# Optimization experiments

Measured on AMD Instinct MI355X. Metric: run time of the kernel, lower is better.

The kernel has to match this reference:

```python
import jax, jax.numpy as jnp
import numpy as np


def setup_inputs() -> dict:
    key = jax.random.key(0)
    ks = jax.random.split(key, 8)
    B, T, C = 4, 1024, 1024
    s = 1.0 / np.sqrt(C)
    return {
        "q": jax.random.normal(ks[0], (B, T, C), jnp.float32),
        "k": jax.random.normal(ks[1], (B, T, C), jnp.float32),
        "v": jax.random.normal(ks[2], (B, T, C), jnp.float32),
        "Wq": jax.random.normal(ks[3], (C, C), jnp.float32) * s,
        "Wk": jax.random.normal(ks[4], (C, C), jnp.float32) * s,
        "Wv": jax.random.normal(ks[5], (C, C), jnp.float32) * s,
        "Wp": jax.random.normal(ks[6], (C, C), jnp.float32) * s,
        "bp": jnp.zeros((C,), jnp.float32),
        "n_head": 16,
        "kernel_size": 16,
    }


def reference(q, k, v, Wq, Wk, Wv, Wp, bp, n_head, kernel_size):
    B, T, C = q.shape
    H = n_head
    D = C // H

    def split_heads(x, W):
        # nn.Linear applies x @ W.T
        return (x @ W.T).reshape(B, T, H, D).transpose(0, 2, 1, 3)  # (B,H,T,D)

    qp = split_heads(q, Wq)
    kp = split_heads(k, Wk)
    vp = split_heads(v, Wv)

    # Faithful to the torch double loop: wei[b,h,i,j] = sum over feature dims
    # d in [max(0, j-ks), min(T, j+ks)) (clipped to [0,D)) of qp[b,h,i,d]*kp[b,h,i,d] / sqrt(D).
    # Both windows index sequence position i; the window slides over the head_dim axis.
    p = qp * kp / jnp.sqrt(jnp.asarray(D, qp.dtype))          # (B,H,T,D)
    cs = jnp.cumsum(p, axis=-1)
    cs = jnp.concatenate([jnp.zeros(cs.shape[:-1] + (1,), cs.dtype), cs], axis=-1)  # (B,H,T,D+1)
    j = jnp.arange(T)
    start = jnp.clip(j - kernel_size, 0, D)                   # (T,)
    end = jnp.clip(jnp.minimum(j + kernel_size, T), 0, D)     # (T,)
    wei = cs[..., end] - cs[..., start]                       # (B,H,T,T): windowed partial dot of row i

    attn = jax.nn.softmax(wei, axis=-1)
    out = jnp.einsum("bhts,bhsd->bhtd", attn, vp)             # (B,H,T,D)
    out = out.transpose(0, 2, 1, 3).reshape(B, T, C)
    out = out @ Wp.T + bp
    # dropout is identity in eval mode
    return out
```

## Files before the change

kernel.cpp:

```cpp
#include <hip/hip_runtime.h>
#include <hip/hip_bf16.h>
#include <stdint.h>


typedef __bf16 bf16x8 __attribute__((ext_vector_type(8)));
typedef float f32x4 __attribute__((ext_vector_type(4)));

#define AS1(p) ((__attribute__((address_space(1))) void*)(p))
#define AS3(p) ((__attribute__((address_space(3))) void*)(p))

__global__ __launch_bounds__(256) void cvt_kernel(
    const float* __restrict__ q, const float* __restrict__ k,
    const float* __restrict__ v, const float* __restrict__ Wq,
    const float* __restrict__ Wk, const float* __restrict__ Wv,
    const float* __restrict__ Wp,
    ushort4* __restrict__ qkv_bf, ushort4* __restrict__ w_bf)
{
  int idx = blockIdx.x * 256 + threadIdx.x;
  const float* src; ushort4* dst; int i;
  if (idx < 3145728) {
    int which = idx >> 20; i = idx & 1048575;
    src = which == 0 ? q : which == 1 ? k : v;
    dst = qkv_bf + (size_t)which * 1048576 + i;
  } else {
    int w = idx - 3145728; int which = w >> 18; i = w & 262143;
    src = which == 0 ? Wq : which == 1 ? Wk : which == 2 ? Wv : Wp;
    dst = w_bf + w;
  }
  float4 val = ((const float4*)src)[i];
  union { ushort4 u; __hip_bfloat16 h[4]; } c;
  c.h[0] = __float2bfloat16(val.x); c.h[1] = __float2bfloat16(val.y);
  c.h[2] = __float2bfloat16(val.z); c.h[3] = __float2bfloat16(val.w);
  dst[0] = c.u;
}

template <typename OutT>
__device__ __forceinline__ void gemm_tile128(
    const __hip_bfloat16* __restrict__ A, const __hip_bfloat16* __restrict__ Bw,
    OutT* __restrict__ C, const float* __restrict__ bias)
{
  const int N = 1024, K = 1024;
  __shared__ __align__(16) __hip_bfloat16 As[2][128 * 32];
  __shared__ __align__(16) __hip_bfloat16 Bs[2][128 * 32];
  const int t = threadIdx.x;
  const int wv = t >> 6, lane = t & 63;
  const int wRow = (wv >> 1) * 64, wCol = (wv & 1) * 64;
  const int mrow = lane & 15, kq = lane >> 4;

  f32x4 acc[4][4] = {};

  for (int k0 = 0; k0 < K; k0 += 64) {
    __syncthreads();
#pragma unroll
    for (int half = 0; half < 2; ++half)
#pragma unroll
      for (int tI = 0; tI < 2; ++tI) {
        int chunk = wv * 2 + tI;
        int byteOff = chunk * 1024 + lane * 16;
        int row = byteOff >> 6;
        int colEl = (byteOff & 63) >> 1;
        const __hip_bfloat16* ga = A + (size_t)row * K + k0 + half * 32 + colEl;
        __builtin_amdgcn_global_load_lds(AS1((void*)ga), AS3(&As[half][chunk * 512]), 16, 0, 0);
        const __hip_bfloat16* gb = Bw + (size_t)row * K + k0 + half * 32 + colEl;
        __builtin_amdgcn_global_load_lds(AS1((void*)gb), AS3(&Bs[half][chunk * 512]), 16, 0, 0);
      }
    __syncthreads();

#pragma unroll
    for (int half = 0; half < 2; ++half) {
      bf16x8 af[4], bf[4];
#pragma unroll
      for (int mi = 0; mi < 4; ++mi)
        af[mi] = *(const bf16x8*)&As[half][(wRow + mi * 16 + mrow) * 32 + kq * 8];
#pragma unroll
      for (int ni = 0; ni < 4; ++ni)
        bf[ni] = *(const bf16x8*)&Bs[half][(wCol + ni * 16 + mrow) * 32 + kq * 8];
#pragma unroll
      for (int mi = 0; mi < 4; ++mi)
#pragma unroll
        for (int ni = 0; ni < 4; ++ni)
          acc[mi][ni] = __builtin_amdgcn_mfma_f32_16x16x32_bf16(af[mi], bf[ni], acc[mi][ni], 0, 0, 0);
    }
  }

#pragma unroll
  for (int mi = 0; mi < 4; ++mi)
#pragma unroll
    for (int ni = 0; ni < 4; ++ni)
#pragma unroll
      for (int r = 0; r < 4; ++r) {
        int row = wRow + mi * 16 + kq * 4 + r;
        int col = wCol + ni * 16 + mrow;
        float val = acc[mi][ni][r];
        if (bias) val += bias[col];
        if constexpr (__is_same(OutT, __hip_bfloat16))
          C[(size_t)row * N + col] = __float2bfloat16(val);
        else
          C[(size_t)row * N + col] = val;
      }
}

__global__ __launch_bounds__(256) void qkv_gemm_kernel(
    const __hip_bfloat16* __restrict__ QKVbf, const __hip_bfloat16* __restrict__ Wbf,
    __hip_bfloat16* __restrict__ QKVp)
{
  int l = blockIdx.x;
  int n = l / 96, mm = l % 96, z = mm >> 5, m = mm & 31;
  gemm_tile128<__hip_bfloat16>(
      QKVbf + (size_t)z * 4194304 + (size_t)m * 131072,
      Wbf + (size_t)z * 1048576 + (size_t)n * 131072,
      QKVp + (size_t)z * 4194304 + (size_t)m * 131072 + n * 128, nullptr);
}

__global__ __launch_bounds__(256) void final_gemm_kernel(
    const __hip_bfloat16* __restrict__ Abf, const __hip_bfloat16* __restrict__ Wpbf,
    float* __restrict__ Out, const float* __restrict__ biasAll)
{
  const int N = 1024, K = 1024;
  int l = blockIdx.x;
  int m = l & 63, n = l >> 6;
  const __hip_bfloat16* A = Abf + (size_t)m * 65536;
  const __hip_bfloat16* Bw = Wpbf + (size_t)n * 131072;
  float* C = Out + (size_t)m * 65536 + n * 128;
  const float* bias = biasAll + n * 128;

  __shared__ __align__(16) __hip_bfloat16 As[2][64 * 32];
  __shared__ __align__(16) __hip_bfloat16 Bs[2][128 * 32];
  const int t = threadIdx.x;
  const int wv = t >> 6, lane = t & 63;
  const int wRow = (wv >> 1) * 32, wCol = (wv & 1) * 64;
  const int mrow = lane & 15, kq = lane >> 4;

  f32x4 acc[2][4] = {};

  for (int k0 = 0; k0 < K; k0 += 64) {
    __syncthreads();
#pragma unroll
    for (int tI = 0; tI < 6; ++tI) {
      int c = wv * 6 + tI;
      int byteOff, row, colEl;
      if (c < 8) {
        int half = c >> 2, ch = c & 3;
        byteOff = ch * 1024 + lane * 16;
        row = byteOff >> 6; colEl = (byteOff & 63) >> 1;
        const __hip_bfloat16* ga = A + (size_t)row * K + k0 + half * 32 + colEl;
        __builtin_amdgcn_global_load_lds(AS1((void*)ga), AS3(&As[half][ch * 512]), 16, 0, 0);
      } else {
        int cb = c - 8, half = cb >> 3, ch = cb & 7;
        byteOff = ch * 1024 + lane * 16;
        row = byteOff >> 6; colEl = (byteOff & 63) >> 1;
        const __hip_bfloat16* gb = Bw + (size_t)row * K + k0 + half * 32 + colEl;
        __builtin_amdgcn_global_load_lds(AS1((void*)gb), AS3(&Bs[half][ch * 512]), 16, 0, 0);
      }
    }
    __syncthreads();

#pragma unroll
    for (int half = 0; half < 2; ++half) {
      bf16x8 af[2], bf[4];
#pragma unroll
      for (int mi = 0; mi < 2; ++mi)
        af[mi] = *(const bf16x8*)&As[half][(wRow + mi * 16 + mrow) * 32 + kq * 8];
#pragma unroll
      for (int ni = 0; ni < 4; ++ni)
        bf[ni] = *(const bf16x8*)&Bs[half][(wCol + ni * 16 + mrow) * 32 + kq * 8];
#pragma unroll
      for (int mi = 0; mi < 2; ++mi)
#pragma unroll
        for (int ni = 0; ni < 4; ++ni)
          acc[mi][ni] = __builtin_amdgcn_mfma_f32_16x16x32_bf16(af[mi], bf[ni], acc[mi][ni], 0, 0, 0);
    }
  }

#pragma unroll
  for (int mi = 0; mi < 2; ++mi)
#pragma unroll
    for (int ni = 0; ni < 4; ++ni)
#pragma unroll
      for (int r = 0; r < 4; ++r) {
        int row = wRow + mi * 16 + kq * 4 + r;
        int col = wCol + ni * 16 + mrow;
        C[(size_t)row * N + col] = acc[mi][ni][r] + bias[col];
      }
}

__global__ __launch_bounds__(256) void tail_partial_kernel(
    const __hip_bfloat16* __restrict__ VP, float* __restrict__ partial)
{
  const int seg = blockIdx.x, bh = blockIdx.y;
  const int b = bh >> 4, h = bh & 15;
  const int d = threadIdx.x & 63, wv = threadIdx.x >> 6;
  const int jBase = 80 + seg * 59;
  float s = 0.0f;
  for (int r = wv; r < 59; r += 4)
    s += __bfloat162float(VP[((size_t)(b * 1024 + jBase + r)) * 1024 + h * 64 + d]);
  __shared__ float red[4][64];
  red[wv][d] = s;
  __syncthreads();
  if (threadIdx.x < 64)
    partial[(bh * 16 + seg) * 64 + threadIdx.x] =
        red[0][threadIdx.x] + red[1][threadIdx.x] + red[2][threadIdx.x] + red[3][threadIdx.x];
}

__global__ __launch_bounds__(256) void attn_kernel(
    const __hip_bfloat16* __restrict__ QP, const __hip_bfloat16* __restrict__ KP,
    const __hip_bfloat16* __restrict__ VP, const float* __restrict__ partial,
    __hip_bfloat16* __restrict__ OUTA)
{
  const int b = blockIdx.z, h = blockIdx.y, i0 = blockIdx.x * 64;
  const int t = threadIdx.x, lane = t & 63, wv = t >> 6;

  __shared__ float csl[64][65];
  __shared__ __align__(16) __hip_bfloat16 wlb[64][96];
  __shared__ __align__(16) __hip_bfloat16 vpt[64][104];
  __shared__ float scl[64], tlw[64], tail[64];

  if (t < 64) {
    const float* pp = partial + (b * 16 + h) * 16 * 64 + t;
    float s = 0.0f;
#pragma unroll
    for (int seg = 0; seg < 16; ++seg) s += pp[seg * 64];
    tail[t] = s;
  }

  for (int idx = t; idx < 80 * 64; idx += 256) {
    int j = idx >> 6, d = idx & 63;
    vpt[d][j] = VP[((size_t)(b * 1024 + j)) * 1024 + h * 64 + d];
  }
  for (int idx = t; idx < 64 * 16; idx += 256) {
    int d = idx >> 4, j = 80 + (idx & 15);
    vpt[d][j] = __float2bfloat16(0.0f);
  }

  for (int ii = 0; ii < 16; ++ii) {
    int i = wv * 16 + ii;
    size_t row = ((size_t)(b * 1024 + i0 + i)) * 1024 + h * 64 + lane;
    float p = __bfloat162float(QP[row]) * __bfloat162float(KP[row]) * 0.125f;
#pragma unroll
    for (int delta = 1; delta < 64; delta <<= 1) {
      float up = __shfl_up(p, (unsigned)delta, 64);
      if (lane >= delta) p += up;
    }
    csl[i][lane] = p;
  }
  __syncthreads();

  {
    int i = t >> 2, jg = t & 3;
    float wloc[20];
    float mx = 0.0f;
#pragma unroll
    for (int q = 0; q < 20; ++q) {
      int j = jg + 4 * q;
      int s = j - 16; s = s < 0 ? 0 : s;
      int e = j + 16; e = e > 64 ? 64 : e;
      float w = csl[i][e - 1] - (s > 0 ? csl[i][s - 1] : 0.0f);
      wloc[q] = w;
      mx = fmaxf(mx, w);
    }
    mx = fmaxf(mx, __shfl_xor(mx, 1, 64));
    mx = fmaxf(mx, __shfl_xor(mx, 2, 64));
    float sum = 0.0f;
#pragma unroll
    for (int q = 0; q < 20; ++q) {
      float e_ = __expf(wloc[q] - mx);
      wlb[i][jg + 4 * q] = __float2bfloat16(e_);
      sum += e_;
    }
#pragma unroll
    for (int q = 0; q < 4; ++q)
      wlb[i][80 + jg + 4 * q] = __float2bfloat16(0.0f);
    sum += __shfl_xor(sum, 1, 64);
    sum += __shfl_xor(sum, 2, 64);
    float tw = __expf(-mx);
    sum += 944.0f * tw;
    if (jg == 0) { scl[i] = 1.0f / sum; tlw[i] = tw / sum; }
  }
  __syncthreads();

  {
    const int mh = (wv >> 1) * 32, nh = (wv & 1) * 32;
    const int mrow = lane & 15, kq = lane >> 4;
    f32x4 acc[2][2] = {};
#pragma unroll
    for (int k0 = 0; k0 < 96; k0 += 32) {
      bf16x8 af[2], bf[2];
#pragma unroll
      for (int mi = 0; mi < 2; ++mi)
        af[mi] = *(const bf16x8*)&wlb[mh + mi * 16 + mrow][k0 + kq * 8];
#pragma unroll
      for (int ni = 0; ni < 2; ++ni)
        bf[ni] = *(const bf16x8*)&vpt[nh + ni * 16 + mrow][k0 + kq * 8];
#pragma unroll
      for (int mi = 0; mi < 2; ++mi)
#pragma unroll
        for (int ni = 0; ni < 2; ++ni)
          acc[mi][ni] = __builtin_amdgcn_mfma_f32_16x16x32_bf16(af[mi], bf[ni], acc[mi][ni], 0, 0, 0);
    }
#pragma unroll
    for (int mi = 0; mi < 2; ++mi)
#pragma unroll
      for (int ni = 0; ni < 2; ++ni)
#pragma unroll
        for (int r = 0; r < 4; ++r) {
          int i = mh + mi * 16 + kq * 4 + r;
          int d = nh + ni * 16 + mrow;
          float o = acc[mi][ni][r] * scl[i] + tlw[i] * tail[d];
          OUTA[((size_t)(b * 1024 + i0 + i)) * 1024 + h * 64 + d] = __float2bfloat16(o);
        }
  }
}

extern "C" void kernel_launch(void* const* d_in, const int* in_sizes, int n_in,
                              void* d_out, int out_size, void* d_ws, size_t ws_size,
                              hipStream_t stream)
{
  (void)in_sizes; (void)n_in; (void)out_size; (void)ws_size;
  const float* q  = (const float*)d_in[0];
  const float* k  = (const float*)d_in[1];
  const float* v  = (const float*)d_in[2];
  const float* Wq = (const float*)d_in[3];
  const float* Wk = (const float*)d_in[4];
  const float* Wv = (const float*)d_in[5];
  const float* Wp = (const float*)d_in[6];
  const float* bp = (const float*)d_in[7];

  char* ws = (char*)d_ws;
  __hip_bfloat16* qkv_bf = (__hip_bfloat16*)(ws);
  __hip_bfloat16* w_bf   = (__hip_bfloat16*)(ws + 25165824);
  __hip_bfloat16* QKVp   = (__hip_bfloat16*)(ws + 33554432);
  __hip_bfloat16* OUTA   = (__hip_bfloat16*)(ws + 58720256);
  float* partial = (float*)(ws);
  float* out = (float*)d_out;

  cvt_kernel<<<dim3(16384), 256, 0, stream>>>(q, k, v, Wq, Wk, Wv, Wp,
      (ushort4*)qkv_bf, (ushort4*)w_bf);
  qkv_gemm_kernel<<<dim3(768), 256, 0, stream>>>(qkv_bf, w_bf, QKVp);
  tail_partial_kernel<<<dim3(16, 64), 256, 0, stream>>>(QKVp + (size_t)2 * 4194304, partial);
  attn_kernel<<<dim3(16, 16, 4), 256, 0, stream>>>(QKVp, QKVp + (size_t)4194304,
                                                   QKVp + (size_t)2 * 4194304, partial, OUTA);
  final_gemm_kernel<<<dim3(512), 256, 0, stream>>>(OUTA, w_bf + (size_t)3 * 1048576,
                                                   out, bp);
}
```

Baseline: 187.4 us.

## Alias csl and vpt in shared memory and vectorize prefix-sum loads

The attention kernel now computes each row's cumulative sum with 16-wide vectorized bf16 loads per thread, doing a serial in-register scan and a 4-lane shuffle for segment offsets. This replaces the 16 iterations of 64-lane shuffle scans per wave. csl and vpt now share one shared-memory buffer, so the VP transpose load is moved after the softmax stage with an extra barrier. This cuts LDS footprint and may raise occupancy, but the VP global load no longer overlaps the prefix-sum phase.

```diff
diff --git a/kernel.cpp b/kernel.cpp
--- a/kernel.cpp
+++ b/kernel.cpp
@@ -210,9 +210,10 @@
   const int b = blockIdx.z, h = blockIdx.y, i0 = blockIdx.x * 64;
   const int t = threadIdx.x, lane = t & 63, wv = t >> 6;
 
-  __shared__ float csl[64][65];
+  __shared__ __align__(16) char bufA[64 * 68 * 4];
+  float (*csl)[68] = (float(*)[68])bufA;
+  __hip_bfloat16 (*vpt)[104] = (__hip_bfloat16(*)[104])bufA;
   __shared__ __align__(16) __hip_bfloat16 wlb[64][96];
-  __shared__ __align__(16) __hip_bfloat16 vpt[64][104];
   __shared__ float scl[64], tlw[64], tail[64];
 
   if (t < 64) {
@@ -223,25 +224,37 @@
     tail[t] = s;
   }
 
-  for (int idx = t; idx < 80 * 64; idx += 256) {
-    int j = idx >> 6, d = idx & 63;
-    vpt[d][j] = VP[((size_t)(b * 1024 + j)) * 1024 + h * 64 + d];
-  }
-  for (int idx = t; idx < 64 * 16; idx += 256) {
-    int d = idx >> 4, j = 80 + (idx & 15);
-    vpt[d][j] = __float2bfloat16(0.0f);
-  }
-
-  for (int ii = 0; ii < 16; ++ii) {
-    int i = wv * 16 + ii;
-    size_t row = ((size_t)(b * 1024 + i0 + i)) * 1024 + h * 64 + lane;
-    float p = __bfloat162float(QP[row]) * __bfloat162float(KP[row]) * 0.125f;
-#pragma unroll
-    for (int delta = 1; delta < 64; delta <<= 1) {
-      float up = __shfl_up(p, (unsigned)delta, 64);
-      if (lane >= delta) p += up;
-    }
-    csl[i][lane] = p;
+  {
+    const int i = t >> 2, seg = t & 3;
+    const size_t base = ((size_t)(b * 1024 + i0 + i)) * 1024 + h * 64 + seg * 16;
+    bf16x8 q0 = *(const bf16x8*)(QP + base);
+    bf16x8 q1 = *(const bf16x8*)(QP + base + 8);
+    bf16x8 k0 = *(const bf16x8*)(KP + base);
+    bf16x8 k1 = *(const bf16x8*)(KP + base + 8);
+    float cs[16];
+    float run = 0.0f;
+#pragma unroll
+    for (int x = 0; x < 8; ++x) {
+      run += (float)q0[x] * (float)k0[x] * 0.125f;
+      cs[x] = run;
+    }
+#pragma unroll
+    for (int x = 0; x < 8; ++x) {
+      run += (float)q1[x] * (float)k1[x] * 0.125f;
+      cs[8 + x] = run;
+    }
+    float t1 = __shfl_up(run, 1, 4);
+    float t2 = __shfl_up(run, 2, 4);
+    float t3 = __shfl_up(run, 3, 4);
+    float off = 0.0f;
+    if (seg > 0) off += t1;
+    if (seg > 1) off += t2;
+    if (seg > 2) off += t3;
+    float4* dst = (float4*)&csl[i][seg * 16];
+#pragma unroll
+    for (int x4 = 0; x4 < 4; ++x4)
+      dst[x4] = make_float4(cs[4 * x4] + off, cs[4 * x4 + 1] + off,
+                            cs[4 * x4 + 2] + off, cs[4 * x4 + 3] + off);
   }
   __syncthreads();
 
@@ -275,6 +288,16 @@
     float tw = __expf(-mx);
     sum += 944.0f * tw;
     if (jg == 0) { scl[i] = 1.0f / sum; tlw[i] = tw / sum; }
+  }
+  __syncthreads();
+
+  for (int idx = t; idx < 80 * 64; idx += 256) {
+    int j = idx >> 6, d = idx & 63;
+    vpt[d][j] = VP[((size_t)(b * 1024 + j)) * 1024 + h * 64 + d];
+  }
+  for (int idx = t; idx < 64 * 16; idx += 256) {
+    int d = idx >> 4, j = 80 + (idx & 15);
+    vpt[d][j] = __float2bfloat16(0.0f);
   }
   __syncthreads();
 
```

Measured after the change: 182.3 us. 2.7% less time.
